# Performance work log

Measured on AMD Instinct MI355X. Metric: run time of the kernel, lower is better.

The kernel has to match this reference:

```python
import jax, jax.numpy as jnp
import numpy as np

WIDTH = 256
FREQS = 10
INPUT_WIDTH = 3 + 3 * 2 * FREQS  # 63


def embed_point(point, freqs):
    # point: [N, 3] -> [N, 3*(1+2*freqs)]
    linear = point[..., None]                                  # [N, 3, 1]
    scales = jnp.exp2(jnp.arange(freqs, dtype=point.dtype))    # [freqs]
    angles = linear * scales                                   # [N, 3, freqs]
    emb = jnp.concatenate((linear, jnp.sin(angles), jnp.cos(angles)), axis=-1)
    return emb.reshape(*point.shape[:-1], 3 * (1 + 2 * freqs))


def _xavier(key, fan_in, fan_out):
    limit = jnp.sqrt(6.0 / (fan_in + fan_out)).astype(jnp.float32)
    return jax.random.uniform(key, (fan_in, fan_out), jnp.float32, -limit, limit)


def setup_inputs() -> dict:
    key = jax.random.key(0)
    keys = jax.random.split(key, 20)
    N = 524288
    point = jax.random.normal(keys[0], (N, 3), dtype=jnp.float32)
    dims = [
        (INPUT_WIDTH, WIDTH), (WIDTH, WIDTH), (WIDTH, WIDTH), (WIDTH, WIDTH),
        (WIDTH, WIDTH), (WIDTH + INPUT_WIDTH, WIDTH), (WIDTH, WIDTH),
        (WIDTH, WIDTH), (WIDTH, 4),
    ]
    inp = {"point": point}
    for i, (fi, fo) in enumerate(dims):
        inp[f"w{i}"] = _xavier(keys[1 + i], fi, fo)
        inp[f"b{i}"] = jnp.zeros((fo,), dtype=jnp.float32)
    return inp


def reference(point, w0, b0, w1, b1, w2, b2, w3, b3, w4, b4,
              w5, b5, w6, b6, w7, b7, w8, b8):
    inp = embed_point(point, FREQS)                 # [N, 63]
    x = jax.nn.relu(inp @ w0 + b0)
    x = jax.nn.relu(x @ w1 + b1)
    x = jax.nn.relu(x @ w2 + b2)
    x = jax.nn.relu(x @ w3 + b3)
    x = jax.nn.relu(x @ w4 + b4)
    x = jax.nn.relu(jnp.concatenate((x, inp), -1) @ w5 + b5)  # skip concat
    x = jax.nn.relu(x @ w6 + b6)
    x = jax.nn.relu(x @ w7 + b7)
    return x @ w8 + b8                              # [N, 4]
```

## Files before the change

kernel.cpp:

```cpp
#include <hip/hip_runtime.h>
#include <math.h>


typedef __attribute__((ext_vector_type(8))) short short8;
typedef __attribute__((ext_vector_type(4))) float f32x4;
typedef __attribute__((ext_vector_type(16))) float f32x16;

struct WPtrs { const float* w[8]; };
struct BPtrs { const float* b[8]; };

#define INV2PI 0.15915494309189533577f

#define PK_L0 0
#define PK_L1 16384
#define PK_L2 81920
#define PK_L3 147456
#define PK_L4 212992
#define PK_L5 278528
#define PK_L6 360448
#define PK_L7 425984
#define PK_W8 491520
#define PK_TOTAL 495616

__device__ __forceinline__ unsigned short f2bf(float v) {
  unsigned u = __float_as_uint(v);
  u = u + 0x7fffu + ((u >> 16) & 1u);
  return (unsigned short)(u >> 16);
}
__device__ __forceinline__ float bf_lo(unsigned u) { return __uint_as_float(u << 16); }
__device__ __forceinline__ float bf_hi(unsigned u) { return __uint_as_float(u & 0xffff0000u); }

__device__ __forceinline__ unsigned cvtpk(float a, float b) {
#if __has_builtin(__builtin_amdgcn_cvt_pk_bf16_f32)
  typedef __attribute__((ext_vector_type(2))) __bf16 bf16x2_t;
  bf16x2_t r = __builtin_amdgcn_cvt_pk_bf16_f32(a, b);
  return __builtin_bit_cast(unsigned, r);
#else
  unsigned ua = __float_as_uint(a);
  ua += 0x7fffu + ((ua >> 16) & 1u);
  unsigned ub = __float_as_uint(b);
  ub += 0x7fffu + ((ub >> 16) & 1u);
#if __has_builtin(__builtin_amdgcn_perm)
  return __builtin_amdgcn_perm(ub, ua, 0x07060302u);
#else
  return (ua >> 16) | (ub & 0xffff0000u);
#endif
#endif
}

__device__ __forceinline__ float fractf_(float x) {
#if __has_builtin(__builtin_amdgcn_fract_f32)
  return __builtin_amdgcn_fract_f32(x);
#else
  return x - floorf(x);
#endif
}
__device__ __forceinline__ float sin_rev(float rev) {
#if __has_builtin(__builtin_amdgcn_sinf)
  return __builtin_amdgcn_sinf(rev);
#else
  return __sinf(rev * 6.283185307179586f);
#endif
}

__device__ __forceinline__ float embval(int f, float c0, float c1, float c2,
                                        float x0, float x1, float x2) {
  if (f >= 63) return 0.0f;
  int d = (f >= 21 ? 1 : 0) + (f >= 42 ? 1 : 0);
  int r = f - d * 21;
  float c = (d == 0) ? c0 : (d == 1 ? c1 : c2);
  float x = (d == 0) ? x0 : (d == 1 ? x1 : x2);
  bool isc = r > 10;
  int e = isc ? (r - 11) : (r - 1);
  float rev = fractf_(ldexpf(x, e) + (isc ? 0.25f : 0.0f));
  float s = sin_rev(rev);
  return (r == 0) ? c : s;
}

__device__ __forceinline__ f32x16 mfma32(short8 a, short8 b, f32x16 c) {
  return __builtin_amdgcn_mfma_f32_32x32x16_bf16(a, b, c, 0, 0, 0);
}
__device__ __forceinline__ f32x4 mfma16(short8 a, short8 b, f32x4 c) {
  return __builtin_amdgcn_mfma_f32_16x16x32_bf16(a, b, c, 0, 0, 0);
}

__global__ void pack_weights(WPtrs W, const float* __restrict__ w8,
                             unsigned short* __restrict__ out) {
  int idx = blockIdx.x * 256 + threadIdx.x;
  if (idx >= PK_TOTAL) return;
  float v;
  if (idx >= PK_W8) {
    int t = idx - PK_W8;
    int j = t >> 8, k = t & 255;
    v = (j < 4) ? w8[k * 4 + j] : 0.0f;
  } else {
    int e = idx & 15;
    int blk = idx >> 4;
    int ch = blk & 255;
    int kkg = blk >> 8;
    int l, kk0;
    if      (kkg < 4)   { l = 0; kk0 = 0;   }
    else if (kkg < 20)  { l = 1; kk0 = 4;   }
    else if (kkg < 36)  { l = 2; kk0 = 20;  }
    else if (kkg < 52)  { l = 3; kk0 = 36;  }
    else if (kkg < 68)  { l = 4; kk0 = 52;  }
    else if (kkg < 88)  { l = 5; kk0 = 68;  }
    else if (kkg < 104) { l = 6; kk0 = 88;  }
    else                { l = 7; kk0 = 104; }
    int k = (kkg - kk0) * 16 + e;
    const int realK[8] = {63, 256, 256, 256, 256, 319, 256, 256};
    v = (k < realK[l]) ? W.w[l][k * 256 + ch] : 0.0f;
  }
  out[idx] = f2bf(v);
}

template <int KKA, int PAB, int KKB, bool RB>
__device__ __forceinline__ void do_layer32(
    const unsigned short* srcA, const unsigned short* srcB,
    const unsigned short* __restrict__ wblk,
    const float* __restrict__ bias,
    unsigned short* dst, int w, int n, int h, unsigned swz) {
  f32x16 acc[2][2];
#pragma unroll
  for (int mt = 0; mt < 2; ++mt)
#pragma unroll
    for (int q = 0; q < 4; ++q) {
      f32x4 bq = *reinterpret_cast<const f32x4*>(bias + w * 64 + mt * 32 + q * 8 + h * 4);
#pragma unroll
      for (int r = 0; r < 4; ++r) {
        acc[mt][0][q * 4 + r] = bq[r];
        acc[mt][1][q * 4 + r] = bq[r];
      }
    }

  const unsigned short* ab = wblk + (unsigned)((w * 64 + n) * 16 + h * 8);
  const char* rA0 = (const char*)srcA + (unsigned)(n * PAB);
  const char* rA1 = rA0 + 32 * PAB;

#pragma unroll 4
  for (int kk = 0; kk < KKA; ++kk) {
    short8 a0 = *reinterpret_cast<const short8*>(ab + kk * 4096);
    short8 a1 = *reinterpret_cast<const short8*>(ab + kk * 4096 + 512);
    unsigned off = ((unsigned)(kk * 32 + h * 16)) ^ swz;
    short8 b0 = *reinterpret_cast<const short8*>(rA0 + off);
    short8 b1 = *reinterpret_cast<const short8*>(rA1 + off);
    acc[0][0] = mfma32(a0, b0, acc[0][0]);
    acc[0][1] = mfma32(a0, b1, acc[0][1]);
    acc[1][0] = mfma32(a1, b0, acc[1][0]);
    acc[1][1] = mfma32(a1, b1, acc[1][1]);
  }
  if (KKB > 0) {
    const char* rB0 = (const char*)srcB + (unsigned)(n * 128);
    const char* rB1 = rB0 + 32 * 128;
#pragma unroll
    for (int kl = 0; kl < KKB; ++kl) {
      const unsigned short* ab2 = ab + (KKA + kl) * 4096;
      short8 a0 = *reinterpret_cast<const short8*>(ab2);
      short8 a1 = *reinterpret_cast<const short8*>(ab2 + 512);
      unsigned off = ((unsigned)(kl * 32 + h * 16)) ^ swz;
      short8 b0 = *reinterpret_cast<const short8*>(rB0 + off);
      short8 b1 = *reinterpret_cast<const short8*>(rB1 + off);
      acc[0][0] = mfma32(a0, b0, acc[0][0]);
      acc[0][1] = mfma32(a0, b1, acc[0][1]);
      acc[1][0] = mfma32(a1, b0, acc[1][0]);
      acc[1][1] = mfma32(a1, b1, acc[1][1]);
    }
  }

  if (RB) __syncthreads();
#pragma unroll
  for (int nt = 0; nt < 2; ++nt) {
    char* rowp = (char*)dst + (unsigned)((nt * 32 + n) * 512);
#pragma unroll
    for (int mt = 0; mt < 2; ++mt)
#pragma unroll
      for (int q = 0; q < 4; ++q) {
        float x0 = fmaxf(acc[mt][nt][q * 4 + 0], 0.0f);
        float x1 = fmaxf(acc[mt][nt][q * 4 + 1], 0.0f);
        float x2 = fmaxf(acc[mt][nt][q * 4 + 2], 0.0f);
        float x3 = fmaxf(acc[mt][nt][q * 4 + 3], 0.0f);
        uint2 pr;
        pr.x = cvtpk(x0, x1);
        pr.y = cvtpk(x2, x3);
        unsigned off = ((unsigned)(w * 128 + mt * 64 + q * 16 + h * 8)) ^ swz;
        *reinterpret_cast<uint2*>(rowp + off) = pr;
      }
  }
  __syncthreads();
}

__launch_bounds__(256, 4)
__global__ void mlp_mfma(const float* __restrict__ pts, long N,
                         BPtrs B, const float* __restrict__ b8,
                         const unsigned short* __restrict__ wpk,
                         float* __restrict__ out) {
  __shared__ unsigned short act[64 * 256];
  __shared__ unsigned short emb[64 * 64];
  const int tid = threadIdx.x;
  const int w = tid >> 6, lane = tid & 63;
  const int n = lane & 31, h = lane >> 5;
  const unsigned swz = (unsigned)((n & 7) << 4);
  const long pbase = (long)blockIdx.x * 64;

  {
    const int pt = tid >> 2, fg = tid & 3;
    const long pg = pbase + pt;
    float c0 = 0.f, c1 = 0.f, c2 = 0.f;
    if (pg < N) {
      const float* pp = pts + pg * 3;
      c0 = pp[0]; c1 = pp[1]; c2 = pp[2];
    }
    float x0 = c0 * INV2PI, x1 = c1 * INV2PI, x2 = c2 * INV2PI;
    unsigned pk[8];
#pragma unroll
    for (int i = 0; i < 16; i += 2) {
      int f0 = fg * 16 + i;
      float v0 = embval(f0,     c0, c1, c2, x0, x1, x2);
      float v1 = embval(f0 + 1, c0, c1, c2, x0, x1, x2);
      pk[i >> 1] = cvtpk(v0, v1);
    }
    const unsigned sw = (unsigned)((pt & 7) << 4);
    char* rowp = (char*)emb + (unsigned)(pt * 128);
    *reinterpret_cast<uint4*>(rowp + (((unsigned)(fg * 32)) ^ sw)) =
        uint4{pk[0], pk[1], pk[2], pk[3]};
    *reinterpret_cast<uint4*>(rowp + (((unsigned)(fg * 32 + 16)) ^ sw)) =
        uint4{pk[4], pk[5], pk[6], pk[7]};
  }
  __syncthreads();

  do_layer32<4,  128, 0, false>(emb, nullptr, wpk + PK_L0, B.b[0], act, w, n, h, swz);
  do_layer32<16, 512, 0, true >(act, nullptr, wpk + PK_L1, B.b[1], act, w, n, h, swz);
  do_layer32<16, 512, 0, true >(act, nullptr, wpk + PK_L2, B.b[2], act, w, n, h, swz);
  do_layer32<16, 512, 0, true >(act, nullptr, wpk + PK_L3, B.b[3], act, w, n, h, swz);
  do_layer32<16, 512, 0, true >(act, nullptr, wpk + PK_L4, B.b[4], act, w, n, h, swz);
  do_layer32<16, 512, 4, true >(act, emb,     wpk + PK_L5, B.b[5], act, w, n, h, swz);
  do_layer32<16, 512, 0, true >(act, nullptr, wpk + PK_L6, B.b[6], act, w, n, h, swz);
  do_layer32<16, 512, 0, true >(act, nullptr, wpk + PK_L7, B.b[7], act, w, n, h, swz);

  {
    const int l16 = lane & 15, quad = lane >> 4;
    const unsigned short* w8b = wpk + PK_W8 + (unsigned)(l16 * 256 + quad * 8);
    const int pt = w * 16 + l16;
    const char* ba = (const char*)act + (unsigned)(pt * 512);
    f32x4 a4 = {0.f, 0.f, 0.f, 0.f};
#pragma unroll
    for (int kk = 0; kk < 8; ++kk) {
      short8 a = *reinterpret_cast<const short8*>(w8b + kk * 32);
      unsigned off = ((unsigned)(kk * 64 + quad * 16)) ^ swz;
      short8 b = *reinterpret_cast<const short8*>(ba + off);
      a4 = mfma16(a, b, a4);
    }
    if (quad == 0) {
      f32x4 bb = *reinterpret_cast<const f32x4*>(b8);
      long pg = pbase + pt;
      f32x4 v = a4 + bb;
      if (pg < N) *reinterpret_cast<f32x4*>(out + pg * 4) = v;
    }
  }
}

__device__ __forceinline__ unsigned pk2s(float a, float b) {
  return (unsigned)f2bf(a) | ((unsigned)f2bf(b) << 16);
}
__device__ __forceinline__ void fb_seg(const unsigned short* src, int kRows,
                                       const float* __restrict__ wr,
                                       int lane, int ps, float acc[4][16]) {
#pragma unroll 4
  for (int k = 0; k < kRows; ++k) {
    const float* p = wr + k * 256 + lane;
    float w0 = p[0], w1 = p[64], w2 = p[128], w3 = p[192];
    const uint4* xr = reinterpret_cast<const uint4*>(src + ((k << 6) + ps));
    uint4 q0 = xr[0], q1 = xr[1];
    float x[16];
    x[0] = bf_lo(q0.x);  x[1] = bf_hi(q0.x);  x[2] = bf_lo(q0.y);  x[3] = bf_hi(q0.y);
    x[4] = bf_lo(q0.z);  x[5] = bf_hi(q0.z);  x[6] = bf_lo(q0.w);  x[7] = bf_hi(q0.w);
    x[8] = bf_lo(q1.x);  x[9] = bf_hi(q1.x);  x[10] = bf_lo(q1.y); x[11] = bf_hi(q1.y);
    x[12] = bf_lo(q1.z); x[13] = bf_hi(q1.z); x[14] = bf_lo(q1.w); x[15] = bf_hi(q1.w);
#pragma unroll
    for (int pp = 0; pp < 16; ++pp) {
      acc[0][pp] = fmaf(w0, x[pp], acc[0][pp]);
      acc[1][pp] = fmaf(w1, x[pp], acc[1][pp]);
      acc[2][pp] = fmaf(w2, x[pp], acc[2][pp]);
      acc[3][pp] = fmaf(w3, x[pp], acc[3][pp]);
    }
  }
}
__device__ __forceinline__ void fb_layer(const unsigned short* srcA, int kA,
                                         const unsigned short* srcB, int kB,
                                         const float* wrA, const float* wrB,
                                         const float* bias,
                                         unsigned short* dst, int lane, int ps) {
  float acc[4][16];
#pragma unroll
  for (int jt = 0; jt < 4; ++jt) {
    float bb = bias[lane + (jt << 6)];
#pragma unroll
    for (int pp = 0; pp < 16; ++pp) acc[jt][pp] = bb;
  }
  fb_seg(srcA, kA, wrA, lane, ps, acc);
  if (srcB) fb_seg(srcB, kB, wrB, lane, ps, acc);
#pragma unroll
  for (int jt = 0; jt < 4; ++jt) {
    unsigned short* dr = dst + (((lane + (jt << 6)) << 6) + ps);
    float r[16];
#pragma unroll
    for (int pp = 0; pp < 16; ++pp) r[pp] = fmaxf(acc[jt][pp], 0.0f);
    uint4 a, b;
    a.x = pk2s(r[0], r[1]);   a.y = pk2s(r[2], r[3]);
    a.z = pk2s(r[4], r[5]);   a.w = pk2s(r[6], r[7]);
    b.x = pk2s(r[8], r[9]);   b.y = pk2s(r[10], r[11]);
    b.z = pk2s(r[12], r[13]); b.w = pk2s(r[14], r[15]);
    reinterpret_cast<uint4*>(dr)[0] = a;
    reinterpret_cast<uint4*>(dr)[1] = b;
  }
}
__launch_bounds__(256, 2)
__global__ void mlp_fallback(const float* __restrict__ pts, int N,
                             WPtrs W, BPtrs B,
                             const float* __restrict__ w8,
                             const float* __restrict__ b8,
                             float* __restrict__ out) {
  __shared__ unsigned short act[256 * 64];
  __shared__ unsigned short emb[64 * 64];
  const int lane = threadIdx.x & 63;
  const int ps = (threadIdx.x >> 6) << 4;
  const long pbase = (long)blockIdx.x * 64 + ps;
#pragma unroll
  for (int i = 0; i < 16; ++i) {
    int idx = (i << 6) + lane;
    int f = idx >> 4, pp = idx & 15;
    float v = 0.0f;
    if (f < 63) {
      float c = (pbase + pp < N) ? pts[(pbase + pp) * 3 + (f / 21)] : 0.0f;
      float x = c * INV2PI;
      v = embval(f, c, c, c, x, x, x);
    }
    emb[(f << 6) + ps + pp] = f2bf(v);
  }
  fb_layer(emb, 63, nullptr, 0, W.w[0], nullptr, B.b[0], act, lane, ps);
#pragma unroll 1
  for (int l = 1; l <= 4; ++l)
    fb_layer(act, 256, nullptr, 0, W.w[l], nullptr, B.b[l], act, lane, ps);
  fb_layer(act, 256, emb, 63, W.w[5], W.w[5] + 256 * 256, B.b[5], act, lane, ps);
#pragma unroll 1
  for (int l = 6; l <= 7; ++l)
    fb_layer(act, 256, nullptr, 0, W.w[l], nullptr, B.b[l], act, lane, ps);
  {
    const int pp = lane & 15, cc = lane >> 4;
    float a = b8[cc];
#pragma unroll 4
    for (int k = 0; k < 256; ++k)
      a = fmaf(bf_lo((unsigned)act[(k << 6) + ps + pp]), w8[(k << 2) + cc], a);
    if (pbase + pp < N) out[(pbase + pp) * 4 + cc] = a;
  }
}

extern "C" void kernel_launch(void* const* d_in, const int* in_sizes, int n_in,
                              void* d_out, int out_size, void* d_ws, size_t ws_size,
                              hipStream_t stream) {
  const float* pts = (const float*)d_in[0];
  WPtrs W; BPtrs B;
  for (int i = 0; i < 8; ++i) {
    W.w[i] = (const float*)d_in[1 + 2 * i];
    B.b[i] = (const float*)d_in[2 + 2 * i];
  }
  const float* w8 = (const float*)d_in[17];
  const float* b8 = (const float*)d_in[18];
  float* out = (float*)d_out;
  const long N = in_sizes[0] / 3;

  const size_t need = (size_t)PK_TOTAL * sizeof(unsigned short);
  if (ws_size >= need) {
    unsigned short* wpk = (unsigned short*)d_ws;
    pack_weights<<<1936, 256, 0, stream>>>(W, w8, wpk);
    mlp_mfma<<<(int)((N + 63) / 64), 256, 0, stream>>>(pts, N, B, b8, wpk, out);
  } else {
    mlp_fallback<<<(int)((N + 63) / 64), 256, 0, stream>>>(pts, (int)N, W, B, w8, b8, out);
  }
}
```

Before: 629.7 us.

## Double point tile per block to 128 for greater weight-fragment reuse

Result: faster. 572.1 us (-9.2%).

```diff
diff --git a/kernel.cpp b/kernel.cpp
--- a/kernel.cpp
+++ b/kernel.cpp
@@ -120,61 +120,76 @@
     const unsigned short* __restrict__ wblk,
     const float* __restrict__ bias,
     unsigned short* dst, int w, int n, int h, unsigned swz) {
-  f32x16 acc[2][2];
+  f32x16 acc[2][4];
 #pragma unroll
   for (int mt = 0; mt < 2; ++mt)
 #pragma unroll
     for (int q = 0; q < 4; ++q) {
       f32x4 bq = *reinterpret_cast<const f32x4*>(bias + w * 64 + mt * 32 + q * 8 + h * 4);
 #pragma unroll
-      for (int r = 0; r < 4; ++r) {
-        acc[mt][0][q * 4 + r] = bq[r];
-        acc[mt][1][q * 4 + r] = bq[r];
-      }
-    }
-
-  const unsigned short* ab = wblk + (unsigned)((w * 64 + n) * 16 + h * 8);
-  const char* rA0 = (const char*)srcA + (unsigned)(n * PAB);
-  const char* rA1 = rA0 + 32 * PAB;
-
-#pragma unroll 4
+      for (int nt = 0; nt < 4; ++nt)
+#pragma unroll
+        for (int r = 0; r < 4; ++r)
+          acc[mt][nt][q * 4 + r] = bq[r];
+    }
+
+  const char* wb = (const char*)wblk;
+  const unsigned aoff = (unsigned)(((w * 64 + n) * 16 + h * 8) * 2);
+  const char* rA = (const char*)srcA + (unsigned)(n * PAB);
+
+#pragma unroll 2
   for (int kk = 0; kk < KKA; ++kk) {
-    short8 a0 = *reinterpret_cast<const short8*>(ab + kk * 4096);
-    short8 a1 = *reinterpret_cast<const short8*>(ab + kk * 4096 + 512);
+    short8 a0 = *reinterpret_cast<const short8*>(wb + (aoff + (unsigned)(kk * 8192)));
+    short8 a1 = *reinterpret_cast<const short8*>(wb + (aoff + (unsigned)(kk * 8192 + 1024)));
     unsigned off = ((unsigned)(kk * 32 + h * 16)) ^ swz;
-    short8 b0 = *reinterpret_cast<const short8*>(rA0 + off);
-    short8 b1 = *reinterpret_cast<const short8*>(rA1 + off);
+    const char* p = rA + off;
+    short8 b0 = *reinterpret_cast<const short8*>(p);
+    short8 b1 = *reinterpret_cast<const short8*>(p + 32 * PAB);
+    short8 b2 = *reinterpret_cast<const short8*>(p + 64 * PAB);
+    short8 b3 = *reinterpret_cast<const short8*>(p + 96 * PAB);
     acc[0][0] = mfma32(a0, b0, acc[0][0]);
     acc[0][1] = mfma32(a0, b1, acc[0][1]);
+    acc[0][2] = mfma32(a0, b2, acc[0][2]);
+    acc[0][3] = mfma32(a0, b3, acc[0][3]);
     acc[1][0] = mfma32(a1, b0, acc[1][0]);
     acc[1][1] = mfma32(a1, b1, acc[1][1]);
+    acc[1][2] = mfma32(a1, b2, acc[1][2]);
+    acc[1][3] = mfma32(a1, b3, acc[1][3]);
   }
   if (KKB > 0) {
-    const char* rB0 = (const char*)srcB + (unsigned)(n * 128);
-    const char* rB1 = rB0 + 32 * 128;
+    const char* rB = (const char*)srcB + (unsigned)(n * 128);
 #pragma unroll
     for (int kl = 0; kl < KKB; ++kl) {
-      const unsigned short* ab2 = ab + (KKA + kl) * 4096;
+      const char* ab2 = wb + (aoff + (unsigned)((KKA + kl) * 8192));
       short8 a0 = *reinterpret_cast<const short8*>(ab2);
-      short8 a1 = *reinterpret_cast<const short8*>(ab2 + 512);
+      short8 a1 = *reinterpret_cast<const short8*>(ab2 + 1024);
       unsigned off = ((unsigned)(kl * 32 + h * 16)) ^ swz;
-      short8 b0 = *reinterpret_cast<const short8*>(rB0 + off);
-      short8 b1 = *reinterpret_cast<const short8*>(rB1 + off);
+      const char* p = rB + off;
+      short8 b0 = *reinterpret_cast<const short8*>(p);
+      short8 b1 = *reinterpret_cast<const short8*>(p + 32 * 128);
+      short8 b2 = *reinterpret_cast<const short8*>(p + 64 * 128);
+      short8 b3 = *reinterpret_cast<const short8*>(p + 96 * 128);
       acc[0][0] = mfma32(a0, b0, acc[0][0]);
       acc[0][1] = mfma32(a0, b1, acc[0][1]);
+      acc[0][2] = mfma32(a0, b2, acc[0][2]);
+      acc[0][3] = mfma32(a0, b3, acc[0][3]);
       acc[1][0] = mfma32(a1, b0, acc[1][0]);
       acc[1][1] = mfma32(a1, b1, acc[1][1]);
+      acc[1][2] = mfma32(a1, b2, acc[1][2]);
+      acc[1][3] = mfma32(a1, b3, acc[1][3]);
     }
   }
 
   if (RB) __syncthreads();
-#pragma unroll
-  for (int nt = 0; nt < 2; ++nt) {
-    char* rowp = (char*)dst + (unsigned)((nt * 32 + n) * 512);
-#pragma unroll
-    for (int mt = 0; mt < 2; ++mt)
-#pragma unroll
-      for (int q = 0; q < 4; ++q) {
+  char* d0 = (char*)dst + (unsigned)(n * 512);
+#pragma unroll
+  for (int mt = 0; mt < 2; ++mt)
+#pragma unroll
+    for (int q = 0; q < 4; ++q) {
+      unsigned soff = ((unsigned)(w * 128 + mt * 64 + q * 16 + h * 8)) ^ swz;
+      char* sp = d0 + soff;
+#pragma unroll
+      for (int nt = 0; nt < 4; ++nt) {
         float x0 = fmaxf(acc[mt][nt][q * 4 + 0], 0.0f);
         float x1 = fmaxf(acc[mt][nt][q * 4 + 1], 0.0f);
         float x2 = fmaxf(acc[mt][nt][q * 4 + 2], 0.0f);
@@ -182,28 +197,28 @@
         uint2 pr;
         pr.x = cvtpk(x0, x1);
         pr.y = cvtpk(x2, x3);
-        unsigned off = ((unsigned)(w * 128 + mt * 64 + q * 16 + h * 8)) ^ swz;
-        *reinterpret_cast<uint2*>(rowp + off) = pr;
+        *reinterpret_cast<uint2*>(sp + nt * 16384) = pr;
       }
-  }
+    }
   __syncthreads();
 }
 
-__launch_bounds__(256, 4)
+__launch_bounds__(256, 2)
 __global__ void mlp_mfma(const float* __restrict__ pts, long N,
                          BPtrs B, const float* __restrict__ b8,
                          const unsigned short* __restrict__ wpk,
                          float* __restrict__ out) {
-  __shared__ unsigned short act[64 * 256];
-  __shared__ unsigned short emb[64 * 64];
+  extern __shared__ unsigned short smem[];
+  unsigned short* act = smem;
+  unsigned short* emb = smem + 32768;
   const int tid = threadIdx.x;
   const int w = tid >> 6, lane = tid & 63;
   const int n = lane & 31, h = lane >> 5;
   const unsigned swz = (unsigned)((n & 7) << 4);
-  const long pbase = (long)blockIdx.x * 64;
+  const long pbase = (long)blockIdx.x * 128;
 
   {
-    const int pt = tid >> 2, fg = tid & 3;
+    const int pt = tid >> 1, fg = tid & 1;
     const long pg = pbase + pt;
     float c0 = 0.f, c1 = 0.f, c2 = 0.f;
     if (pg < N) {
@@ -211,20 +226,24 @@
       c0 = pp[0]; c1 = pp[1]; c2 = pp[2];
     }
     float x0 = c0 * INV2PI, x1 = c1 * INV2PI, x2 = c2 * INV2PI;
-    unsigned pk[8];
-#pragma unroll
-    for (int i = 0; i < 16; i += 2) {
-      int f0 = fg * 16 + i;
-      float v0 = embval(f0,     c0, c1, c2, x0, x1, x2);
-      float v1 = embval(f0 + 1, c0, c1, c2, x0, x1, x2);
-      pk[i >> 1] = cvtpk(v0, v1);
-    }
     const unsigned sw = (unsigned)((pt & 7) << 4);
     char* rowp = (char*)emb + (unsigned)(pt * 128);
-    *reinterpret_cast<uint4*>(rowp + (((unsigned)(fg * 32)) ^ sw)) =
-        uint4{pk[0], pk[1], pk[2], pk[3]};
-    *reinterpret_cast<uint4*>(rowp + (((unsigned)(fg * 32 + 16)) ^ sw)) =
-        uint4{pk[4], pk[5], pk[6], pk[7]};
+#pragma unroll
+    for (int jb = 0; jb < 2; ++jb) {
+      unsigned pk[8];
+#pragma unroll
+      for (int i = 0; i < 16; i += 2) {
+        int f0 = fg * 32 + jb * 16 + i;
+        float v0 = embval(f0,     c0, c1, c2, x0, x1, x2);
+        float v1 = embval(f0 + 1, c0, c1, c2, x0, x1, x2);
+        pk[i >> 1] = cvtpk(v0, v1);
+      }
+      unsigned base = (unsigned)(fg * 64 + jb * 32);
+      *reinterpret_cast<uint4*>(rowp + (base ^ sw)) =
+          uint4{pk[0], pk[1], pk[2], pk[3]};
+      *reinterpret_cast<uint4*>(rowp + ((base + 16) ^ sw)) =
+          uint4{pk[4], pk[5], pk[6], pk[7]};
+    }
   }
   __syncthreads();
 
@@ -240,21 +259,27 @@
   {
     const int l16 = lane & 15, quad = lane >> 4;
     const unsigned short* w8b = wpk + PK_W8 + (unsigned)(l16 * 256 + quad * 8);
-    const int pt = w * 16 + l16;
-    const char* ba = (const char*)act + (unsigned)(pt * 512);
-    f32x4 a4 = {0.f, 0.f, 0.f, 0.f};
-#pragma unroll
-    for (int kk = 0; kk < 8; ++kk) {
-      short8 a = *reinterpret_cast<const short8*>(w8b + kk * 32);
-      unsigned off = ((unsigned)(kk * 64 + quad * 16)) ^ swz;
-      short8 b = *reinterpret_cast<const short8*>(ba + off);
-      a4 = mfma16(a, b, a4);
-    }
-    if (quad == 0) {
-      f32x4 bb = *reinterpret_cast<const f32x4*>(b8);
-      long pg = pbase + pt;
-      f32x4 v = a4 + bb;
-      if (pg < N) *reinterpret_cast<f32x4*>(out + pg * 4) = v;
+    short8 wf[8];
+#pragma unroll
+    for (int kk = 0; kk < 8; ++kk)
+      wf[kk] = *reinterpret_cast<const short8*>(w8b + kk * 32);
+    f32x4 bb = *reinterpret_cast<const f32x4*>(b8);
+#pragma unroll
+    for (int it = 0; it < 2; ++it) {
+      const int pt = w * 32 + it * 16 + l16;
+      const char* ba = (const char*)act + (unsigned)(pt * 512);
+      f32x4 a4 = {0.f, 0.f, 0.f, 0.f};
+#pragma unroll
+      for (int kk = 0; kk < 8; ++kk) {
+        unsigned off = ((unsigned)(kk * 64 + quad * 16)) ^ swz;
+        short8 b = *reinterpret_cast<const short8*>(ba + off);
+        a4 = mfma16(wf[kk], b, a4);
+      }
+      if (quad == 0) {
+        long pg = pbase + pt;
+        f32x4 v = a4 + bb;
+        if (pg < N) *reinterpret_cast<f32x4*>(out + pg * 4) = v;
+      }
     }
   }
 }
@@ -371,10 +396,15 @@
 
   const size_t need = (size_t)PK_TOTAL * sizeof(unsigned short);
   if (ws_size >= need) {
-    unsigned short* wpk = (unsigned short*)d_ws;
-    pack_weights<<<1936, 256, 0, stream>>>(W, w8, wpk);
-    mlp_mfma<<<(int)((N + 63) / 64), 256, 0, stream>>>(pts, N, B, b8, wpk, out);
-  } else {
-    mlp_fallback<<<(int)((N + 63) / 64), 256, 0, stream>>>(pts, (int)N, W, B, w8, b8, out);
-  }
-}
+    static hipError_t attr_err = hipFuncSetAttribute(
+        reinterpret_cast<const void*>(mlp_mfma),
+        hipFuncAttributeMaxDynamicSharedMemorySize, 81920);
+    if (attr_err == hipSuccess) {
+      unsigned short* wpk = (unsigned short*)d_ws;
+      pack_weights<<<1936, 256, 0, stream>>>(W, w8, wpk);
+      mlp_mfma<<<(int)((N + 127) / 128), 256, 81920, stream>>>(pts, N, B, b8, wpk, out);
+      return;
+    }
+  }
+  mlp_fallback<<<(int)((N + 63) / 64), 256, 0, stream>>>(pts, (int)N, W, B, w8, b8, out);
+}
```
